# Kernel tuning notes

Measured on AMD Instinct MI355X. Metric: run time of the kernel, lower is better.

The kernel has to match this reference:

```python
import jax, jax.numpy as jnp
import numpy as np

MIX_TIME = 20
NUM_SAMPLES = 128
NUM_ONES = 64


def setup_inputs() -> dict:
    key = jax.random.key(0)
    kz, ka, kw = jax.random.split(key, 3)
    B, D, DZ = 128, 512, 512
    z = (jax.random.uniform(kz, (B, DZ)) < 0.5).astype(jnp.float32)  # conditioned binary vars
    A = jax.random.normal(ka, (D, D), dtype=jnp.float32) * 0.02      # pairwise couplings
    W = jax.random.normal(kw, (D, DZ), dtype=jnp.float32) * 0.02     # w-z couplings
    return {"z": z, "A": A, "W": W}


def reference(z, A, W):
    # Batched conditional double-flip Gibbs sampler.
    # State x: (S, B, D) binary floats; per step pick distinct coords (i, j),
    # evaluate unnormalized log p(w|z) for the 4 value combos, sample categorically.
    S = NUM_SAMPLES
    B, DZ = z.shape
    D = A.shape[0]

    x0 = jnp.zeros((S, B, D), dtype=jnp.float32).at[..., :NUM_ONES].set(1.0)
    cond = jnp.broadcast_to(z[None], (S, B, DZ))  # (S,B,DZ)

    def logp(w):  # quadratic energy: w^T A w + w^T W z  -> (S,B)
        return (jnp.einsum('sbd,de,sbe->sb', w, A, w)
                + jnp.einsum('sbd,dk,sbk->sb', w, W, cond))

    combos = jnp.array([[0., 0.], [0., 1.], [1., 0.], [1., 1.]], dtype=jnp.float32)

    def step(x, k):
        ki, ks = jax.random.split(k)
        ij = jax.random.choice(ki, D, (2,), replace=False)  # distinct i, j
        i, j = ij[0], ij[1]

        def set_ij(v):  # clone x with coords (i,j) set to (v0, v1)
            return x.at[..., i].set(v[0]).at[..., j].set(v[1])

        xs = jax.vmap(set_ij)(combos)                    # (4,S,B,D)
        logits = jnp.moveaxis(jax.vmap(logp)(xs), 0, -1)  # (S,B,4)
        samp = jax.random.categorical(ks, logits)         # (S,B) in {0,1,2,3}
        iv = (samp // 2).astype(x.dtype)
        jv = (samp % 2).astype(x.dtype)
        x = x.at[..., i].set(iv).at[..., j].set(jv)
        return x, None

    keys = jax.random.split(jax.random.key(1), MIX_TIME)
    x, _ = jax.lax.scan(step, x0, keys)
    return x
```

## Files before the change

### kernel.cpp

```cpp
#include <hip/hip_runtime.h>
#include <stdint.h>

#define MIX_TIME 20
#define NCHAIN   16384
#define DDIM     512

#define WS_TBL 0
#define WS_SC  128
#define WS_T0  288
#define WS_U0  800
#define WS_G   1312
#define WS_GT  2912
#define WS_ST0 4512
#define WS_SZ0 4544
#define WS_C   4672

struct U2 { uint32_t a, b; };

__device__ __forceinline__ uint32_t rotl32(uint32_t v, int r) {
  return (v << r) | (v >> (32 - r));
}

__device__ __forceinline__ U2 tf2x32(uint32_t k0, uint32_t k1, uint32_t x0, uint32_t x1) {
  const uint32_t ks2 = k0 ^ k1 ^ 0x1BD11BDAu;
  x0 += k0; x1 += k1;
  x0 += x1; x1 = rotl32(x1, 13); x1 ^= x0;
  x0 += x1; x1 = rotl32(x1, 15); x1 ^= x0;
  x0 += x1; x1 = rotl32(x1, 26); x1 ^= x0;
  x0 += x1; x1 = rotl32(x1,  6); x1 ^= x0;
  x0 += k1; x1 += ks2 + 1u;
  x0 += x1; x1 = rotl32(x1, 17); x1 ^= x0;
  x0 += x1; x1 = rotl32(x1, 29); x1 ^= x0;
  x0 += x1; x1 = rotl32(x1, 16); x1 ^= x0;
  x0 += x1; x1 = rotl32(x1, 24); x1 ^= x0;
  x0 += ks2; x1 += k0 + 2u;
  x0 += x1; x1 = rotl32(x1, 13); x1 ^= x0;
  x0 += x1; x1 = rotl32(x1, 15); x1 ^= x0;
  x0 += x1; x1 = rotl32(x1, 26); x1 ^= x0;
  x0 += x1; x1 = rotl32(x1,  6); x1 ^= x0;
  x0 += k0; x1 += k1 + 3u;
  x0 += x1; x1 = rotl32(x1, 17); x1 ^= x0;
  x0 += x1; x1 = rotl32(x1, 29); x1 ^= x0;
  x0 += x1; x1 = rotl32(x1, 16); x1 ^= x0;
  x0 += x1; x1 = rotl32(x1, 24); x1 ^= x0;
  x0 += k1; x1 += ks2 + 4u;
  x0 += x1; x1 = rotl32(x1, 13); x1 ^= x0;
  x0 += x1; x1 = rotl32(x1, 15); x1 ^= x0;
  x0 += x1; x1 = rotl32(x1, 26); x1 ^= x0;
  x0 += x1; x1 = rotl32(x1,  6); x1 ^= x0;
  x0 += ks2; x1 += k0 + 5u;
  return {x0, x1};
}

__device__ __forceinline__ uint32_t rbits32(uint32_t k0, uint32_t k1, uint32_t m) {
  U2 r = tf2x32(k0, k1, 0u, m);
  return r.a ^ r.b;
}
__device__ __forceinline__ U2 split_key(uint32_t k0, uint32_t k1, uint32_t idx) {
  return tf2x32(k0, k1, 0u, idx);
}

__device__ __forceinline__ float gumbel_from(uint32_t bits) {
  float u = __uint_as_float(0x3f800000u | (bits >> 9)) - 1.0f;
  u = fmaxf(u + 1.17549435e-38f, 1.17549435e-38f);
  return -logf(-logf(u));
}

__device__ __forceinline__ float bpermf(int byteidx, float v) {
  return __int_as_float(__builtin_amdgcn_ds_bpermute(byteidx, __float_as_int(v)));
}
__device__ __forceinline__ uint32_t bpermu(int byteidx, uint32_t v) {
  return (uint32_t)__builtin_amdgcn_ds_bpermute(byteidx, (int)v);
}

__global__ __launch_bounds__(256)
void pre_kernel(const float* __restrict__ A, const float* __restrict__ W,
                const float* __restrict__ z, uint32_t* __restrict__ wsu,
                float* __restrict__ wsf) {
  const int bid = blockIdx.x, tid = threadIdx.x;
  uint32_t* tbl = wsu + WS_TBL;
  uint32_t* sc  = wsu + WS_SC;
  float* T0  = wsf + WS_T0;
  float* U0  = wsf + WS_U0;
  float* G   = wsf + WS_G;
  float* Gt  = wsf + WS_GT;
  float* St0 = wsf + WS_ST0;
  float* Sz0 = wsf + WS_SZ0;
  float* C   = wsf + WS_C;

  __shared__ uint32_t tblL[4 * MIX_TIME];
  __shared__ float    sred[64];
  __shared__ float4   zs4[128];

  if (bid == 0) {
    const int wv = tid >> 6;
    const uint32_t lane = (uint32_t)(tid & 63);
    #pragma unroll 1
    for (int k5 = 0; k5 < 5; ++k5) {
      const uint32_t t = (uint32_t)(wv * 5 + k5);
      const U2 K   = split_key(0u, 1u, t);
      const U2 ki  = split_key(K.a, K.b, 0u);
      const U2 ks  = split_key(K.a, K.b, 1u);
      const U2 sub = split_key(ki.a, ki.b, 1u);

      uint32_t k1 = 0xFFFFFFFFu, m1 = 0xFFFFFFFFu;
      uint32_t k2 = 0xFFFFFFFFu, m2 = 0xFFFFFFFFu;
      #pragma unroll
      for (int p = 0; p < 8; ++p) {
        const uint32_t m   = lane + 64u * (uint32_t)p;
        const uint32_t key = rbits32(sub.a, sub.b, m);
        const bool lt1 = (key < k1) || (key == k1 && m < m1);
        const bool lt2 = (key < k2) || (key == k2 && m < m2);
        if (lt1)      { k2 = k1; m2 = m1; k1 = key; m1 = m; }
        else if (lt2) { k2 = key; m2 = m; }
      }
      #pragma unroll
      for (int msk = 1; msk < 64; msk <<= 1) {
        const uint32_t ok1 = __shfl_xor((int)k1, msk, 64);
        const uint32_t om1 = __shfl_xor((int)m1, msk, 64);
        const uint32_t ok2 = __shfl_xor((int)k2, msk, 64);
        const uint32_t om2 = __shfl_xor((int)m2, msk, 64);
        const bool oless = (ok1 < k1) || (ok1 == k1 && om1 < m1);
        if (oless) {
          const bool l2 = (k1 < ok2) || (k1 == ok2 && m1 < om2);
          const uint32_t nk2 = l2 ? k1 : ok2, nm2 = l2 ? m1 : om2;
          k1 = ok1; m1 = om1; k2 = nk2; m2 = nm2;
        } else {
          const bool l2 = (ok1 < k2) || (ok1 == k2 && om1 < m2);
          if (l2) { k2 = ok1; m2 = om1; }
        }
      }
      if (lane == 0) {
        tbl[4u * t + 0u] = m1;  tblL[4u * t + 0u] = m1;
        tbl[4u * t + 1u] = m2;  tblL[4u * t + 1u] = m2;
        tbl[4u * t + 2u] = ks.a; tblL[4u * t + 2u] = ks.a;
        tbl[4u * t + 3u] = ks.b; tblL[4u * t + 3u] = ks.b;
      }
    }
    __syncthreads();
    if (tid < MIX_TIME) {
      const uint32_t i = tblL[4 * tid], j = tblL[4 * tid + 1];
      uint32_t* s = sc + 8 * tid;
      s[0] = i; s[1] = j;
      s[2] = __float_as_uint(A[(size_t)i * DDIM + i]);
      s[3] = __float_as_uint(A[(size_t)i * DDIM + j]);
      s[4] = __float_as_uint(A[(size_t)j * DDIM + i]);
      s[5] = __float_as_uint(A[(size_t)j * DDIM + j]);
      s[6] = 0u; s[7] = 0u;
    }
    #pragma unroll 1
    for (int p = tid; p < 1600; p += 256) {
      const int r = p / 40, c = p % 40;
      const uint32_t cr = tblL[4 * (r >> 1) + (r & 1)];
      const uint32_t cc = tblL[4 * (c >> 1) + (c & 1)];
      G[p]  = A[(size_t)cr * DDIM + cc];
      Gt[p] = A[(size_t)cc * DDIM + cr];
    }
    return;
  }

  if (bid <= 2) {
    const int e = (bid - 1) * 256 + tid;
    float s = 0.f;
    #pragma unroll 1
    for (int d = 0; d < 64; ++d) s += A[(size_t)d * DDIM + e];
    T0[e] = s;
    if (bid == 1) {
      if (tid < 64) sred[tid] = s;
      __syncthreads();
      if (tid == 0) {
        float q = 0.f;
        #pragma unroll 1
        for (int e2 = 0; e2 < 64; ++e2) q += sred[e2];
        St0[0] = q;
      }
    }
    return;
  }

  if (bid <= 4) {
    const int d = (bid - 3) * 256 + tid;
    const float4* Ar = reinterpret_cast<const float4*>(A + (size_t)d * DDIM);
    float s = 0.f;
    #pragma unroll
    for (int k = 0; k < 16; ++k) {
      const float4 v = Ar[k];
      s += v.x; s += v.y; s += v.z; s += v.w;
    }
    U0[d] = s;
    return;
  }

  const int cb = bid - 5;
  const int b = cb >> 2, slab = cb & 3;
  if (tid < 128) zs4[tid] = reinterpret_cast<const float4*>(z + (size_t)b * DDIM)[tid];
  __syncthreads();
  if (tid < 128) {
    const int d = slab * 128 + tid;
    const float4* Wr = reinterpret_cast<const float4*>(W + (size_t)d * DDIM);
    float s = 0.f;
    #pragma unroll 4
    for (int k = 0; k < 128; ++k) {
      const float4 w = Wr[k], zz = zs4[k];
      s = fmaf(w.x, zz.x, s); s = fmaf(w.y, zz.y, s);
      s = fmaf(w.z, zz.z, s); s = fmaf(w.w, zz.w, s);
    }
    C[(size_t)b * DDIM + d] = s;
    if (slab == 0 && tid < 64) sred[tid] = s;
  }
  __syncthreads();
  if (slab == 0 && tid == 0) {
    float s = 0.f;
    #pragma unroll 1
    for (int e = 0; e < 64; ++e) s += sred[e];
    Sz0[b] = s;
  }
}

__global__ __launch_bounds__(256)
void gibbs8_kernel(const uint32_t* __restrict__ wsu,
                   const float* __restrict__ wsf,
                   float* __restrict__ out) {
  const int tid = threadIdx.x;
  const int l = tid & 63, wv = tid >> 6;
  const uint32_t* tbl = wsu + WS_TBL;
  const uint32_t* sc  = wsu + WS_SC;
  const float* T0w  = wsf + WS_T0;
  const float* U0w  = wsf + WS_U0;
  const float* Gg   = wsf + WS_G;
  const float* St0w = wsf + WS_ST0;
  const float* Sz0w = wsf + WS_SZ0;
  const float* Cw   = wsf + WS_C;

  __shared__ __align__(16) float gg[3200];
  #pragma unroll
  for (int k = 0; k < 4; ++k) {
    const int idx = tid + k * 256;
    if (idx < 800)
      reinterpret_cast<float4*>(gg)[idx] = reinterpret_cast<const float4*>(Gg)[idx];
  }

  const int ql = l >> 3, qs = l & 7, c4 = l & 3;
  const uint32_t chainbase = ((uint32_t)blockIdx.x * 4u + (uint32_t)wv) * 8u;
  const uint32_t chain_l = chainbase + (uint32_t)ql;
  const uint32_t b_l = chain_l & 127u;
  const uint32_t b_s = (chainbase + (uint32_t)qs) & 127u;
  const float fa  = (float)((c4 >> 1) & 1);
  const float fb  = (float)(c4 & 1);
  const float fab = fa * fb;

  float fTi[3], fTj[3], fUi[3], fUj[3], fci[3], fcj[3], fxi[3], fxj[3];
  uint32_t iiK[3], jjK[3];
  const float* ggb[3];
  #pragma unroll
  for (int k = 0; k < 3; ++k) {
    const int tp = (64 * k + l) >> 3;
    const int tc = (tp < MIX_TIME) ? tp : 0;
    const uint32_t i = sc[8 * tc], j = sc[8 * tc + 1];
    iiK[k] = i; jjK[k] = j;
    fTi[k] = T0w[i];  fTj[k] = T0w[j];
    fUi[k] = U0w[i];  fUj[k] = U0w[j];
    fci[k] = Cw[(size_t)b_s * DDIM + i];
    fcj[k] = Cw[(size_t)b_s * DDIM + j];
    fxi[k] = (i < 64u) ? 1.f : 0.f;
    fxj[k] = (j < 64u) ? 1.f : 0.f;
    ggb[k] = &gg[2 * tc];
  }
  float St = St0w[0];
  float Sz = Sz0w[b_l];
  uint32_t mlo = (qs == 0) ? 0xFFFFFFFFu : 0u;
  uint32_t mhi = mlo;

  float garr[10];
  #pragma unroll
  for (int k = 0; k < 10; ++k) {
    const int f = 64 * k + l;
    const int t = f >> 5;
    const uint32_t qg = ((uint32_t)l & 31u) >> 2;
    const uint32_t m  = (chainbase + qg) * 4u + (uint32_t)(l & 3);
    garr[k] = gumbel_from(rbits32(tbl[4 * t + 2], tbl[4 * t + 3], m));
  }
  __syncthreads();

  const int gvbase = (4 * ql + c4) << 2;
  const int bq4    = ql << 2;

  #pragma unroll
  for (int t = 0; t < MIX_TIME; ++t) {
    const int kS   = t >> 3;
    const int bidx = (((8 * t) & 63) << 2) + bq4;
    const float Ti  = bpermf(bidx, fTi[kS]);
    const float Tj  = bpermf(bidx, fTj[kS]);
    const float Ui  = bpermf(bidx, fUi[kS]);
    const float Uj  = bpermf(bidx, fUj[kS]);
    const float cib = bpermf(bidx, fci[kS]);
    const float cjb = bpermf(bidx, fcj[kS]);
    const float xi  = bpermf(bidx, fxi[kS]);
    const float xj  = bpermf(bidx, fxj[kS]);
    const float gv  = bpermf(gvbase + ((t & 1) << 7), garr[t >> 1]);

    const uint32_t ii = sc[8 * t], jj = sc[8 * t + 1];
    const float Aii = __uint_as_float(sc[8 * t + 2]);
    const float Aij = __uint_as_float(sc[8 * t + 3]);
    const float Aji = __uint_as_float(sc[8 * t + 4]);
    const float Ajj = __uint_as_float(sc[8 * t + 5]);

    const float si   = Ui - xi * Aii - xj * Aij;
    const float sj   = Uj - xi * Aji - xj * Ajj;
    const float sTR  = St - xi * Ti - xj * Tj;
    const float szR  = Sz - xi * cib - xj * cjb;
    const float QR   = sTR - xi * si - xj * sj;
    const float coli = Ti - xi * Aii - xj * Aji;
    const float colj = Tj - xi * Aij - xj * Ajj;
    const float base = QR + szR;
    const float gi   = si + coli + Aii + cib;
    const float gj   = sj + colj + Ajj + cjb;
    const float gij  = Aij + Aji;
    const float v    = gv + (base + fa * gi + fb * gj + fab * gij);

    float bv = v; int bestc = c4;
    #pragma unroll
    for (int msk = 1; msk < 4; msk <<= 1) {
      const float ov = __shfl_xor(bv, msk, 64);
      const int   oc = __shfl_xor(bestc, msk, 64);
      if (ov > bv || (ov == bv && oc < bestc)) { bv = ov; bestc = oc; }
    }

    const int ian = (bestc >> 1) & 1, ibn = bestc & 1;
    const float fan = (float)ian, fbn = (float)ibn;
    const float fdi = fan - xi, fdj = fbn - xj;

    St = St + fdi * Ti + fdj * Tj
            + fdi * (si + fan * Aii + fbn * Aij)
            + fdj * (sj + fan * Aji + fbn * Ajj);
    Sz = Sz + fdi * cib + fdj * cjb;

    const int pk  = ((int)fdi + 1) | (((int)fdj + 1) << 2) | (bestc << 4);
    const int pks = __builtin_amdgcn_ds_bpermute(qs << 5, pk);
    const float fdi_s = (float)((pks & 3) - 1);
    const float fdj_s = (float)(((pks >> 2) & 3) - 1);
    const float fan_s = (float)((pks >> 5) & 1);
    const float fbn_s = (float)((pks >> 4) & 1);

    #pragma unroll
    for (int k = 0; k < 3; ++k) {
      const float2 ga = *reinterpret_cast<const float2*>(ggb[k] + 80 * t);
      const float2 gB = *reinterpret_cast<const float2*>(ggb[k] + 80 * t + 40);
      const float2 gc = *reinterpret_cast<const float2*>(ggb[k] + 1600 + 80 * t);
      const float2 gd = *reinterpret_cast<const float2*>(ggb[k] + 1600 + 80 * t + 40);
      fTi[k] = fmaf(fdi_s, ga.x, fmaf(fdj_s, gB.x, fTi[k]));
      fTj[k] = fmaf(fdi_s, ga.y, fmaf(fdj_s, gB.y, fTj[k]));
      fUi[k] = fmaf(fdi_s, gc.x, fmaf(fdj_s, gd.x, fUi[k]));
      fUj[k] = fmaf(fdi_s, gc.y, fmaf(fdj_s, gd.y, fUj[k]));
      fxi[k] = (iiK[k] == ii) ? fan_s : fxi[k];
      fxi[k] = (iiK[k] == jj) ? fbn_s : fxi[k];
      fxj[k] = (jjK[k] == ii) ? fan_s : fxj[k];
      fxj[k] = (jjK[k] == jj) ? fbn_s : fxj[k];
    }

    {
      const uint32_t ib = 1u << (ii & 31u);
      const uint32_t nv = (uint32_t)(-(int)ian) & ib;
      const bool own_i = ((uint32_t)qs == (ii >> 6));
      if ((ii >> 5) & 1u) { if (own_i) mhi = (mhi & ~ib) | nv; }
      else                { if (own_i) mlo = (mlo & ~ib) | nv; }
      const uint32_t jb = 1u << (jj & 31u);
      const uint32_t nj = (uint32_t)(-(int)ibn) & jb;
      const bool own_j = ((uint32_t)qs == (jj >> 6));
      if ((jj >> 5) & 1u) { if (own_j) mhi = (mhi & ~jb) | nj; }
      else                { if (own_j) mlo = (mlo & ~jb) | nj; }
    }
  }

  {
    float* wavebase = out + (size_t)chainbase * DDIM;
    #pragma unroll
    for (int g = 0; g < 16; ++g) {
      const int bidx = 16 * g + ((l >> 4) << 2);
      const uint32_t wlo = bpermu(bidx, mlo);
      const uint32_t whi = bpermu(bidx, mhi);
      const uint32_t w   = ((l >> 3) & 1) ? whi : wlo;
      const uint32_t nib = (w >> (4 * (l & 7))) & 0xFu;
      float4 o;
      o.x = (float)( nib       & 1u);
      o.y = (float)((nib >> 1) & 1u);
      o.z = (float)((nib >> 2) & 1u);
      o.w = (float)((nib >> 3) & 1u);
      *reinterpret_cast<float4*>(
          wavebase + (size_t)((g >> 1) * 512 + (64 * (g & 1) + l) * 4)) = o;
    }
  }
}

extern "C" void kernel_launch(void* const* d_in, const int* in_sizes, int n_in,
                              void* d_out, int out_size, void* d_ws, size_t ws_size,
                              hipStream_t stream) {
  const float* z = (const float*)d_in[0];
  const float* A = (const float*)d_in[1];
  const float* W = (const float*)d_in[2];
  float* out = (float*)d_out;
  uint32_t* wsu = (uint32_t*)d_ws;
  float*    wsf = (float*)d_ws;

  hipLaunchKernelGGL(pre_kernel, dim3(5 + 512), dim3(256), 0, stream,
                     A, W, z, wsu, wsf);
  hipLaunchKernelGGL(gibbs8_kernel, dim3(NCHAIN / 32), dim3(256), 0, stream,
                     wsu, wsf, out);
}
```

Measured before the change: 51.63 us.

## Parallelize coordinate-pair selection across blocks and gather G tiles inside Gibbs kernel

```diff
diff --git a/kernel.cpp b/kernel.cpp
--- a/kernel.cpp
+++ b/kernel.cpp
@@ -9,11 +9,9 @@
 #define WS_SC  128
 #define WS_T0  288
 #define WS_U0  800
-#define WS_G   1312
-#define WS_GT  2912
-#define WS_ST0 4512
-#define WS_SZ0 4544
-#define WS_C   4672
+#define WS_ST0 1312
+#define WS_SZ0 1344
+#define WS_C   1472
 
 struct U2 { uint32_t a, b; };
 
@@ -82,90 +80,75 @@
   uint32_t* sc  = wsu + WS_SC;
   float* T0  = wsf + WS_T0;
   float* U0  = wsf + WS_U0;
-  float* G   = wsf + WS_G;
-  float* Gt  = wsf + WS_GT;
   float* St0 = wsf + WS_ST0;
   float* Sz0 = wsf + WS_SZ0;
   float* C   = wsf + WS_C;
 
-  __shared__ uint32_t tblL[4 * MIX_TIME];
-  __shared__ float    sred[64];
-  __shared__ float4   zs4[128];
-
-  if (bid == 0) {
-    const int wv = tid >> 6;
-    const uint32_t lane = (uint32_t)(tid & 63);
-    #pragma unroll 1
-    for (int k5 = 0; k5 < 5; ++k5) {
-      const uint32_t t = (uint32_t)(wv * 5 + k5);
-      const U2 K   = split_key(0u, 1u, t);
-      const U2 ki  = split_key(K.a, K.b, 0u);
-      const U2 ks  = split_key(K.a, K.b, 1u);
-      const U2 sub = split_key(ki.a, ki.b, 1u);
-
-      uint32_t k1 = 0xFFFFFFFFu, m1 = 0xFFFFFFFFu;
-      uint32_t k2 = 0xFFFFFFFFu, m2 = 0xFFFFFFFFu;
-      #pragma unroll
-      for (int p = 0; p < 8; ++p) {
-        const uint32_t m   = lane + 64u * (uint32_t)p;
-        const uint32_t key = rbits32(sub.a, sub.b, m);
-        const bool lt1 = (key < k1) || (key == k1 && m < m1);
-        const bool lt2 = (key < k2) || (key == k2 && m < m2);
-        if (lt1)      { k2 = k1; m2 = m1; k1 = key; m1 = m; }
-        else if (lt2) { k2 = key; m2 = m; }
+  __shared__ float  sred[64];
+  __shared__ float4 zs4[8][128];
+  __shared__ float  credL[8][64];
+
+  if (bid < MIX_TIME) {
+    if (tid >= 64) return;
+    const uint32_t t    = (uint32_t)bid;
+    const uint32_t lane = (uint32_t)tid;
+    const U2 K   = split_key(0u, 1u, t);
+    const U2 ki  = split_key(K.a, K.b, 0u);
+    const U2 ks  = split_key(K.a, K.b, 1u);
+    const U2 sub = split_key(ki.a, ki.b, 1u);
+
+    uint32_t k1 = 0xFFFFFFFFu, m1 = 0xFFFFFFFFu;
+    uint32_t k2 = 0xFFFFFFFFu, m2 = 0xFFFFFFFFu;
+    #pragma unroll
+    for (int p = 0; p < 8; ++p) {
+      const uint32_t m   = lane + 64u * (uint32_t)p;
+      const uint32_t key = rbits32(sub.a, sub.b, m);
+      const bool lt1 = (key < k1) || (key == k1 && m < m1);
+      const bool lt2 = (key < k2) || (key == k2 && m < m2);
+      if (lt1)      { k2 = k1; m2 = m1; k1 = key; m1 = m; }
+      else if (lt2) { k2 = key; m2 = m; }
+    }
+    #pragma unroll
+    for (int msk = 1; msk < 64; msk <<= 1) {
+      const uint32_t ok1 = __shfl_xor((int)k1, msk, 64);
+      const uint32_t om1 = __shfl_xor((int)m1, msk, 64);
+      const uint32_t ok2 = __shfl_xor((int)k2, msk, 64);
+      const uint32_t om2 = __shfl_xor((int)m2, msk, 64);
+      const bool oless = (ok1 < k1) || (ok1 == k1 && om1 < m1);
+      if (oless) {
+        const bool l2 = (k1 < ok2) || (k1 == ok2 && m1 < om2);
+        const uint32_t nk2 = l2 ? k1 : ok2, nm2 = l2 ? m1 : om2;
+        k1 = ok1; m1 = om1; k2 = nk2; m2 = nm2;
+      } else {
+        const bool l2 = (ok1 < k2) || (ok1 == k2 && om1 < m2);
+        if (l2) { k2 = ok1; m2 = om1; }
       }
-      #pragma unroll
-      for (int msk = 1; msk < 64; msk <<= 1) {
-        const uint32_t ok1 = __shfl_xor((int)k1, msk, 64);
-        const uint32_t om1 = __shfl_xor((int)m1, msk, 64);
-        const uint32_t ok2 = __shfl_xor((int)k2, msk, 64);
-        const uint32_t om2 = __shfl_xor((int)m2, msk, 64);
-        const bool oless = (ok1 < k1) || (ok1 == k1 && om1 < m1);
-        if (oless) {
-          const bool l2 = (k1 < ok2) || (k1 == ok2 && m1 < om2);
-          const uint32_t nk2 = l2 ? k1 : ok2, nm2 = l2 ? m1 : om2;
-          k1 = ok1; m1 = om1; k2 = nk2; m2 = nm2;
-        } else {
-          const bool l2 = (ok1 < k2) || (ok1 == k2 && om1 < m2);
-          if (l2) { k2 = ok1; m2 = om1; }
-        }
-      }
-      if (lane == 0) {
-        tbl[4u * t + 0u] = m1;  tblL[4u * t + 0u] = m1;
-        tbl[4u * t + 1u] = m2;  tblL[4u * t + 1u] = m2;
-        tbl[4u * t + 2u] = ks.a; tblL[4u * t + 2u] = ks.a;
-        tbl[4u * t + 3u] = ks.b; tblL[4u * t + 3u] = ks.b;
-      }
-    }
-    __syncthreads();
-    if (tid < MIX_TIME) {
-      const uint32_t i = tblL[4 * tid], j = tblL[4 * tid + 1];
-      uint32_t* s = sc + 8 * tid;
-      s[0] = i; s[1] = j;
-      s[2] = __float_as_uint(A[(size_t)i * DDIM + i]);
-      s[3] = __float_as_uint(A[(size_t)i * DDIM + j]);
-      s[4] = __float_as_uint(A[(size_t)j * DDIM + i]);
-      s[5] = __float_as_uint(A[(size_t)j * DDIM + j]);
-      s[6] = 0u; s[7] = 0u;
-    }
-    #pragma unroll 1
-    for (int p = tid; p < 1600; p += 256) {
-      const int r = p / 40, c = p % 40;
-      const uint32_t cr = tblL[4 * (r >> 1) + (r & 1)];
-      const uint32_t cc = tblL[4 * (c >> 1) + (c & 1)];
-      G[p]  = A[(size_t)cr * DDIM + cc];
-      Gt[p] = A[(size_t)cc * DDIM + cr];
+    }
+    if (lane == 0) {
+      tbl[4u * t + 0u] = m1;
+      tbl[4u * t + 1u] = m2;
+      tbl[4u * t + 2u] = ks.a;
+      tbl[4u * t + 3u] = ks.b;
+      sc[8u * t + 0u] = m1;
+      sc[8u * t + 1u] = m2;
+      sc[8u * t + 6u] = 0u;
+      sc[8u * t + 7u] = 0u;
+    }
+    if (lane < 4) {
+      const uint32_t r = (lane < 2) ? m1 : m2;
+      const uint32_t c = (lane & 1) ? m2 : m1;
+      sc[8u * t + 2u + lane] = __float_as_uint(A[(size_t)r * DDIM + c]);
     }
     return;
   }
 
-  if (bid <= 2) {
-    const int e = (bid - 1) * 256 + tid;
+  if (bid <= MIX_TIME + 1) {
+    const int e = (bid - MIX_TIME) * 256 + tid;
     float s = 0.f;
     #pragma unroll 1
     for (int d = 0; d < 64; ++d) s += A[(size_t)d * DDIM + e];
     T0[e] = s;
-    if (bid == 1) {
+    if (bid == MIX_TIME) {
       if (tid < 64) sred[tid] = s;
       __syncthreads();
       if (tid == 0) {
@@ -178,8 +161,8 @@
     return;
   }
 
-  if (bid <= 4) {
-    const int d = (bid - 3) * 256 + tid;
+  if (bid <= MIX_TIME + 3) {
+    const int d = (bid - MIX_TIME - 2) * 256 + tid;
     const float4* Ar = reinterpret_cast<const float4*>(A + (size_t)d * DDIM);
     float s = 0.f;
     #pragma unroll
@@ -191,34 +174,44 @@
     return;
   }
 
-  const int cb = bid - 5;
-  const int b = cb >> 2, slab = cb & 3;
-  if (tid < 128) zs4[tid] = reinterpret_cast<const float4*>(z + (size_t)b * DDIM)[tid];
+  const int cb = bid - (MIX_TIME + 4);
+  const int bg = cb >> 3, slab = cb & 7;
+  #pragma unroll
+  for (int k = 0; k < 4; ++k) {
+    const int idx = tid + 256 * k;
+    const int br = idx >> 7, c4i = idx & 127;
+    zs4[br][c4i] = reinterpret_cast<const float4*>(z + (size_t)(bg * 8 + br) * DDIM)[c4i];
+  }
   __syncthreads();
-  if (tid < 128) {
-    const int d = slab * 128 + tid;
-    const float4* Wr = reinterpret_cast<const float4*>(W + (size_t)d * DDIM);
-    float s = 0.f;
-    #pragma unroll 4
-    for (int k = 0; k < 128; ++k) {
-      const float4 w = Wr[k], zz = zs4[k];
-      s = fmaf(w.x, zz.x, s); s = fmaf(w.y, zz.y, s);
-      s = fmaf(w.z, zz.z, s); s = fmaf(w.w, zz.w, s);
-    }
-    C[(size_t)b * DDIM + d] = s;
-    if (slab == 0 && tid < 64) sred[tid] = s;
-  }
+  const int r = tid & 63;
+  const int h = tid >> 6;
+  const int d = slab * 64 + r;
+  const float4* Wr = reinterpret_cast<const float4*>(W + (size_t)d * DDIM);
+  float s0 = 0.f, s1 = 0.f;
+  #pragma unroll 4
+  for (int k = 0; k < 128; ++k) {
+    const float4 w = Wr[k];
+    const float4 za = zs4[2 * h][k], zb = zs4[2 * h + 1][k];
+    s0 = fmaf(w.x, za.x, s0); s0 = fmaf(w.y, za.y, s0);
+    s0 = fmaf(w.z, za.z, s0); s0 = fmaf(w.w, za.w, s0);
+    s1 = fmaf(w.x, zb.x, s1); s1 = fmaf(w.y, zb.y, s1);
+    s1 = fmaf(w.z, zb.z, s1); s1 = fmaf(w.w, zb.w, s1);
+  }
+  C[(size_t)(bg * 8 + 2 * h) * DDIM + d]     = s0;
+  C[(size_t)(bg * 8 + 2 * h + 1) * DDIM + d] = s1;
+  if (slab == 0) { credL[2 * h][r] = s0; credL[2 * h + 1][r] = s1; }
   __syncthreads();
-  if (slab == 0 && tid == 0) {
+  if (slab == 0 && tid < 8) {
     float s = 0.f;
     #pragma unroll 1
-    for (int e = 0; e < 64; ++e) s += sred[e];
-    Sz0[b] = s;
+    for (int e = 0; e < 64; ++e) s += credL[tid][e];
+    Sz0[bg * 8 + tid] = s;
   }
 }
 
 __global__ __launch_bounds__(256)
-void gibbs8_kernel(const uint32_t* __restrict__ wsu,
+void gibbs8_kernel(const float* __restrict__ A,
+                   const uint32_t* __restrict__ wsu,
                    const float* __restrict__ wsf,
                    float* __restrict__ out) {
   const int tid = threadIdx.x;
@@ -227,17 +220,21 @@
   const uint32_t* sc  = wsu + WS_SC;
   const float* T0w  = wsf + WS_T0;
   const float* U0w  = wsf + WS_U0;
-  const float* Gg   = wsf + WS_G;
   const float* St0w = wsf + WS_ST0;
   const float* Sz0w = wsf + WS_SZ0;
   const float* Cw   = wsf + WS_C;
 
   __shared__ __align__(16) float gg[3200];
-  #pragma unroll
-  for (int k = 0; k < 4; ++k) {
-    const int idx = tid + k * 256;
-    if (idx < 800)
-      reinterpret_cast<float4*>(gg)[idx] = reinterpret_cast<const float4*>(Gg)[idx];
+  __shared__ uint32_t tblL[80];
+  if (tid < 80) tblL[tid] = tbl[tid];
+  __syncthreads();
+  #pragma unroll 1
+  for (int p = tid; p < 1600; p += 256) {
+    const int r = p / 40, c = p % 40;
+    const uint32_t cr = tblL[4 * (r >> 1) + (r & 1)];
+    const uint32_t cc = tblL[4 * (c >> 1) + (c & 1)];
+    gg[p]        = A[(size_t)cr * DDIM + cc];
+    gg[1600 + p] = A[(size_t)cc * DDIM + cr];
   }
 
   const int ql = l >> 3, qs = l & 7, c4 = l & 3;
@@ -344,18 +341,20 @@
 
     #pragma unroll
     for (int k = 0; k < 3; ++k) {
-      const float2 ga = *reinterpret_cast<const float2*>(ggb[k] + 80 * t);
-      const float2 gB = *reinterpret_cast<const float2*>(ggb[k] + 80 * t + 40);
-      const float2 gc = *reinterpret_cast<const float2*>(ggb[k] + 1600 + 80 * t);
-      const float2 gd = *reinterpret_cast<const float2*>(ggb[k] + 1600 + 80 * t + 40);
-      fTi[k] = fmaf(fdi_s, ga.x, fmaf(fdj_s, gB.x, fTi[k]));
-      fTj[k] = fmaf(fdi_s, ga.y, fmaf(fdj_s, gB.y, fTj[k]));
-      fUi[k] = fmaf(fdi_s, gc.x, fmaf(fdj_s, gd.x, fUi[k]));
-      fUj[k] = fmaf(fdi_s, gc.y, fmaf(fdj_s, gd.y, fUj[k]));
-      fxi[k] = (iiK[k] == ii) ? fan_s : fxi[k];
-      fxi[k] = (iiK[k] == jj) ? fbn_s : fxi[k];
-      fxj[k] = (jjK[k] == ii) ? fan_s : fxj[k];
-      fxj[k] = (jjK[k] == jj) ? fbn_s : fxj[k];
+      if (t < 8 * k + 7) {
+        const float2 ga = *reinterpret_cast<const float2*>(ggb[k] + 80 * t);
+        const float2 gB = *reinterpret_cast<const float2*>(ggb[k] + 80 * t + 40);
+        const float2 gc = *reinterpret_cast<const float2*>(ggb[k] + 1600 + 80 * t);
+        const float2 gd = *reinterpret_cast<const float2*>(ggb[k] + 1600 + 80 * t + 40);
+        fTi[k] = fmaf(fdi_s, ga.x, fmaf(fdj_s, gB.x, fTi[k]));
+        fTj[k] = fmaf(fdi_s, ga.y, fmaf(fdj_s, gB.y, fTj[k]));
+        fUi[k] = fmaf(fdi_s, gc.x, fmaf(fdj_s, gd.x, fUi[k]));
+        fUj[k] = fmaf(fdi_s, gc.y, fmaf(fdj_s, gd.y, fUj[k]));
+        fxi[k] = (iiK[k] == ii) ? fan_s : fxi[k];
+        fxi[k] = (iiK[k] == jj) ? fbn_s : fxi[k];
+        fxj[k] = (jjK[k] == ii) ? fan_s : fxj[k];
+        fxj[k] = (jjK[k] == jj) ? fbn_s : fxj[k];
+      }
     }
 
     {
@@ -402,8 +401,8 @@
   uint32_t* wsu = (uint32_t*)d_ws;
   float*    wsf = (float*)d_ws;
 
-  hipLaunchKernelGGL(pre_kernel, dim3(5 + 512), dim3(256), 0, stream,
+  hipLaunchKernelGGL(pre_kernel, dim3(MIX_TIME + 4 + 128), dim3(256), 0, stream,
                      A, W, z, wsu, wsf);
   hipLaunchKernelGGL(gibbs8_kernel, dim3(NCHAIN / 32), dim3(256), 0, stream,
-                     wsu, wsf, out);
-}
+                     A, wsu, wsf, out);
+}
```

Measured after the change: 51.87 us. No clear change (+0.5%).
